# Kernel optimization log

Measured on AMD Instinct MI355X. Metric: run time of the kernel, lower is better.

The kernel has to match this reference:

```python
import jax, jax.numpy as jnp
import numpy as np

OUT = 7   # output_size
SR = 2    # sampling_ratio
SCALES = (0.25, 0.125, 0.0625, 0.03125)  # inferred from feat sizes vs 800x800 image
K_MIN, LVL0, S0, EPS = 2, 4.0, 224.0, 1e-6


def _bilinear_gather(feat, b, y, x):
    """Legacy (aligned=False) bilinear sampling. feat [B,C,H,W]; b,y,x same shape S.
    Returns [*S, C]."""
    B, C, H, W = feat.shape
    valid = (y >= -1.0) & (y <= H) & (x >= -1.0) & (x <= W)
    y = jnp.maximum(y, 0.0)
    x = jnp.maximum(x, 0.0)
    yl = y.astype(jnp.int32)
    xl = x.astype(jnp.int32)
    ycond = yl >= H - 1
    yl = jnp.where(ycond, H - 1, yl)
    yh = jnp.where(ycond, H - 1, yl + 1)
    y = jnp.where(ycond, yl.astype(y.dtype), y)
    xcond = xl >= W - 1
    xl = jnp.where(xcond, W - 1, xl)
    xh = jnp.where(xcond, W - 1, xl + 1)
    x = jnp.where(xcond, xl.astype(x.dtype), x)
    ly = y - yl
    lx = x - xl
    hy = 1.0 - ly
    hx = 1.0 - lx
    def g(yy, xx):
        return feat[b, :, yy, xx]  # advanced indexing -> [*S, C]
    val = ((hy * hx)[..., None] * g(yl, xl)
           + (hy * lx)[..., None] * g(yl, xh)
           + (ly * hx)[..., None] * g(yh, xl)
           + (ly * lx)[..., None] * g(yh, xh))
    return jnp.where(valid[..., None], val, 0.0)


def _roi_align(feat, bidx, boxes, scale):
    """RoIAlign (aligned=False). feat [B,C,H,W], bidx [R] int, boxes [R,4] image coords.
    Returns [R,C,OUT,OUT]."""
    x1 = boxes[:, 0] * scale
    y1 = boxes[:, 1] * scale
    x2 = boxes[:, 2] * scale
    y2 = boxes[:, 3] * scale
    roi_w = jnp.maximum(x2 - x1, 1.0)
    roi_h = jnp.maximum(y2 - y1, 1.0)
    bin_h = roi_h / OUT
    bin_w = roi_w / OUT
    off = (jnp.arange(SR, dtype=feat.dtype) + 0.5) / SR      # [SR]
    ph = jnp.arange(OUT, dtype=feat.dtype)                   # [OUT]
    grid = ph[None, :, None] + off[None, None, :]            # [1,OUT,SR]
    ys = y1[:, None, None] + grid * bin_h[:, None, None]     # [R,OUT,SR]
    xs = x1[:, None, None] + grid * bin_w[:, None, None]     # [R,OUT,SR]
    Y = ys[:, :, None, :, None]                              # [R,OUT,1,SR,1]
    X = xs[:, None, :, None, :]                              # [R,1,OUT,1,SR]
    Yb, Xb = jnp.broadcast_arrays(Y, X)                      # [R,OUT,OUT,SR,SR]
    b = jnp.broadcast_to(bidx[:, None, None, None, None], Yb.shape)
    val = _bilinear_gather(feat, b, Yb, Xb)                  # [R,OUT,OUT,SR,SR,C]
    pooled = val.mean(axis=(3, 4))                           # [R,OUT,OUT,C]
    return jnp.transpose(pooled, (0, 3, 1, 2))               # [R,C,OUT,OUT]


def _levels(boxes_flat):
    """LevelMapper.run: FPN level index (0-based) per RoI."""
    area = (boxes_flat[:, 2] - boxes_flat[:, 0]) * (boxes_flat[:, 3] - boxes_flat[:, 1])
    s = jnp.sqrt(area)
    lvl = jnp.floor(LVL0 + jnp.log2(s / S0 + EPS))
    return jnp.clip(lvl, K_MIN, K_MIN + 3).astype(jnp.int32) - K_MIN


def setup_inputs() -> dict:
    key = jax.random.key(0)
    ks = jax.random.split(key, 6)
    sizes = [200, 100, 50, 25]
    inp = {f"feat{i}": jax.random.normal(ks[i], (2, 256, s, s), dtype=jnp.float32)
           for i, s in enumerate(sizes)}
    xy = jax.random.uniform(ks[4], (2, 256, 2), dtype=jnp.float32) * 500.0
    wh = jax.random.uniform(ks[5], (2, 256, 2), dtype=jnp.float32) * 400.0 + 8.0
    inp["boxes"] = jnp.concatenate([xy, xy + wh], axis=-1)  # (x1,y1,x2,y2) in [0,908)
    return inp


def reference(feat0, feat1, feat2, feat3, boxes):
    feats = [feat0, feat1, feat2, feat3]
    B, N, _ = boxes.shape
    bf = boxes.reshape(B * N, 4)
    bidx = jnp.repeat(jnp.arange(B, dtype=jnp.int32), N)  # convert_to_roi_format ids
    lv = _levels(bf)
    C = feats[0].shape[1]
    out = jnp.zeros((B * N, C, OUT, OUT), dtype=feats[0].dtype)
    for level, (f, sc) in enumerate(zip(feats, SCALES)):
        r = _roi_align(f, bidx, bf, sc)
        out = jnp.where((lv == level)[:, None, None, None], r, out)
    return out
```

## Files before the change

kernel.cpp:

```cpp
#include <hip/hip_runtime.h>

#define OUT 7
#define SR 2
#define NCH 256
#define NB 2
#define NPER 256
#define NROI (NB * NPER)

struct RoiMeta {
    int   level;
    int   bidx;
    float x1, y1;
    float bin_w, bin_h;
};

__global__ void roi_meta_kernel(const float* __restrict__ boxes,
                                RoiMeta* __restrict__ meta) {
    int r = blockIdx.x * blockDim.x + threadIdx.x;
    if (r >= NROI) return;
    float bx1 = boxes[r * 4 + 0];
    float by1 = boxes[r * 4 + 1];
    float bx2 = boxes[r * 4 + 2];
    float by2 = boxes[r * 4 + 3];

    float area = (bx2 - bx1) * (by2 - by1);
    float s    = sqrtf(area);
    float lvl  = floorf(4.0f + log2f(s / 224.0f + 1e-6f));
    lvl        = fminf(fmaxf(lvl, 2.0f), 5.0f);
    int level  = (int)lvl - 2;

    float scale = 0.25f / (float)(1 << level);
    float x1 = bx1 * scale;
    float y1 = by1 * scale;
    float x2 = bx2 * scale;
    float y2 = by2 * scale;
    float roi_w = fmaxf(x2 - x1, 1.0f);
    float roi_h = fmaxf(y2 - y1, 1.0f);

    RoiMeta m;
    m.level = level;
    m.bidx  = r / NPER;
    m.x1    = x1;
    m.y1    = y1;
    m.bin_w = roi_w * (1.0f / OUT);
    m.bin_h = roi_h * (1.0f / OUT);
    meta[r] = m;
}

__device__ __forceinline__ float bilinear_legacy(const float* __restrict__ plane,
                                                 int H, int W, float y, float x) {
    bool valid = (y >= -1.0f) && (y <= (float)H) && (x >= -1.0f) && (x <= (float)W);
    y = fmaxf(y, 0.0f);
    x = fmaxf(x, 0.0f);
    int yl = (int)y;
    int xl = (int)x;
    int yh, xh;
    if (yl >= H - 1) { yl = H - 1; yh = H - 1; y = (float)yl; }
    else             { yh = yl + 1; }
    if (xl >= W - 1) { xl = W - 1; xh = W - 1; x = (float)xl; }
    else             { xh = xl + 1; }
    float ly = y - (float)yl;
    float lx = x - (float)xl;
    float hy = 1.0f - ly;
    float hx = 1.0f - lx;
    const float* rowl = plane + (size_t)yl * W;
    const float* rowh = plane + (size_t)yh * W;
    float v = hy * hx * rowl[xl] + hy * lx * rowl[xh]
            + ly * hx * rowh[xl] + ly * lx * rowh[xh];
    return valid ? v : 0.0f;
}

__global__ void roi_align_kernel(const float* __restrict__ f0,
                                 const float* __restrict__ f1,
                                 const float* __restrict__ f2,
                                 const float* __restrict__ f3,
                                 const RoiMeta* __restrict__ meta,
                                 float* __restrict__ out) {
    int idx = blockIdx.x * blockDim.x + threadIdx.x;
    int pw = idx % OUT;
    int t  = idx / OUT;
    int ph = t % OUT;
    t /= OUT;
    int c = t % NCH;
    int r = t / NCH;
    if (r >= NROI) return;

    RoiMeta m = meta[r];
    const float* f;
    int H;
    switch (m.level) {
        case 0:  f = f0; H = 200; break;
        case 1:  f = f1; H = 100; break;
        case 2:  f = f2; H = 50;  break;
        default: f = f3; H = 25;  break;
    }
    int W = H;
    const float* plane = f + ((size_t)m.bidx * NCH + (size_t)c) * (size_t)H * (size_t)W;

    float acc = 0.0f;
#pragma unroll
    for (int iy = 0; iy < SR; ++iy) {
        float yy = m.y1 + ((float)ph + ((float)iy + 0.5f) * (1.0f / SR)) * m.bin_h;
#pragma unroll
        for (int ix = 0; ix < SR; ++ix) {
            float xx = m.x1 + ((float)pw + ((float)ix + 0.5f) * (1.0f / SR)) * m.bin_w;
            acc += bilinear_legacy(plane, H, W, yy, xx);
        }
    }
    out[idx] = acc * (1.0f / (SR * SR));
}

extern "C" void kernel_launch(void* const* d_in, const int* in_sizes, int n_in,
                              void* d_out, int out_size, void* d_ws, size_t ws_size,
                              hipStream_t stream) {
    const float* f0    = (const float*)d_in[0];
    const float* f1    = (const float*)d_in[1];
    const float* f2    = (const float*)d_in[2];
    const float* f3    = (const float*)d_in[3];
    const float* boxes = (const float*)d_in[4];
    float* out         = (float*)d_out;
    RoiMeta* meta      = (RoiMeta*)d_ws;

    roi_meta_kernel<<<(NROI + 255) / 256, 256, 0, stream>>>(boxes, meta);

    const long long total = (long long)NROI * NCH * OUT * OUT;
    const int block = 256;
    const long long grid = (total + block - 1) / block;
    roi_align_kernel<<<(int)grid, block, 0, stream>>>(f0, f1, f2, f3, meta, out);
}
```

Before: 213.8 us.

## Fuse ROI metadata into align kernel with XCD-aware block mapping and batched loads

Removes the separate metadata kernel and computes each ROI's level, scale and bin sizes inline from the box coordinates, made wave-uniform with readfirstlane. Blocks are remapped so that all blocks of one ROI land on the same XCD (block index mod 8), which should improve L2 reuse of that ROI's feature region. Each block now covers exactly one ROI (TPR divisible by 256). Bilinear weights and offsets are precomputed and all 16 gathers are issued before accumulation to raise memory-level parallelism. Costs are redundant box math per thread and the assumption that the hardware dispatches blocks round-robin across XCDs.

```diff
diff --git a/kernel.cpp b/kernel.cpp
--- a/kernel.cpp
+++ b/kernel.cpp
@@ -1,113 +1,110 @@
 #include <hip/hip_runtime.h>
 
 #define OUT 7
-#define SR 2
 #define NCH 256
 #define NB 2
 #define NPER 256
 #define NROI (NB * NPER)
+#define TPR (NCH * OUT * OUT)
+#define BPR (TPR / 256)
 
-struct RoiMeta {
-    int   level;
-    int   bidx;
-    float x1, y1;
-    float bin_w, bin_h;
-};
+__device__ __forceinline__ float rfl_f(float v) {
+    return __int_as_float(__builtin_amdgcn_readfirstlane(__float_as_int(v)));
+}
 
-__global__ void roi_meta_kernel(const float* __restrict__ boxes,
-                                RoiMeta* __restrict__ meta) {
-    int r = blockIdx.x * blockDim.x + threadIdx.x;
-    if (r >= NROI) return;
-    float bx1 = boxes[r * 4 + 0];
-    float by1 = boxes[r * 4 + 1];
-    float bx2 = boxes[r * 4 + 2];
-    float by2 = boxes[r * 4 + 3];
+__global__ __launch_bounds__(256) void roi_align_kernel(
+        const float* __restrict__ f0, const float* __restrict__ f1,
+        const float* __restrict__ f2, const float* __restrict__ f3,
+        const float* __restrict__ boxes, float* __restrict__ out) {
+    int b    = blockIdx.x;
+    int xcd  = b & 7;
+    int slot = b >> 3;
+    int rr   = slot / BPR;
+    int j    = slot - rr * BPR;
+    int r    = (rr << 3) | xcd;
+
+    int lin = j * 256 + (int)threadIdx.x;
+    int pw  = lin % OUT;
+    int t   = lin / OUT;
+    int ph  = t % OUT;
+    int c   = t / OUT;
+
+    float bx1 = rfl_f(boxes[r * 4 + 0]);
+    float by1 = rfl_f(boxes[r * 4 + 1]);
+    float bx2 = rfl_f(boxes[r * 4 + 2]);
+    float by2 = rfl_f(boxes[r * 4 + 3]);
 
     float area = (bx2 - bx1) * (by2 - by1);
     float s    = sqrtf(area);
-    float lvl  = floorf(4.0f + log2f(s / 224.0f + 1e-6f));
+    float lvl  = floorf(4.0f + log2f(s * (1.0f / 224.0f) + 1e-6f));
     lvl        = fminf(fmaxf(lvl, 2.0f), 5.0f);
-    int level  = (int)lvl - 2;
+    int level  = __builtin_amdgcn_readfirstlane((int)lvl - 2);
 
-    float scale = 0.25f / (float)(1 << level);
+    const float* f;
+    int H;
+    float scale;
+    switch (level) {
+        case 0:  f = f0; H = 200; scale = 0.25f;    break;
+        case 1:  f = f1; H = 100; scale = 0.125f;   break;
+        case 2:  f = f2; H = 50;  scale = 0.0625f;  break;
+        default: f = f3; H = 25;  scale = 0.03125f; break;
+    }
+    float Hf = (float)H;
+
     float x1 = bx1 * scale;
     float y1 = by1 * scale;
-    float x2 = bx2 * scale;
-    float y2 = by2 * scale;
-    float roi_w = fmaxf(x2 - x1, 1.0f);
-    float roi_h = fmaxf(y2 - y1, 1.0f);
+    float roi_w = fmaxf(bx2 * scale - x1, 1.0f);
+    float roi_h = fmaxf(by2 * scale - y1, 1.0f);
+    float bin_w = roi_w * (1.0f / OUT);
+    float bin_h = roi_h * (1.0f / OUT);
 
-    RoiMeta m;
-    m.level = level;
-    m.bidx  = r / NPER;
-    m.x1    = x1;
-    m.y1    = y1;
-    m.bin_w = roi_w * (1.0f / OUT);
-    m.bin_h = roi_h * (1.0f / OUT);
-    meta[r] = m;
-}
+    int bidx = r >> 8;
+    const float* plane = f + (size_t)(bidx * NCH + c) * (size_t)(H * H);
 
-__device__ __forceinline__ float bilinear_legacy(const float* __restrict__ plane,
-                                                 int H, int W, float y, float x) {
-    bool valid = (y >= -1.0f) && (y <= (float)H) && (x >= -1.0f) && (x <= (float)W);
-    y = fmaxf(y, 0.0f);
-    x = fmaxf(x, 0.0f);
-    int yl = (int)y;
-    int xl = (int)x;
-    int yh, xh;
-    if (yl >= H - 1) { yl = H - 1; yh = H - 1; y = (float)yl; }
-    else             { yh = yl + 1; }
-    if (xl >= W - 1) { xl = W - 1; xh = W - 1; x = (float)xl; }
-    else             { xh = xl + 1; }
-    float ly = y - (float)yl;
-    float lx = x - (float)xl;
-    float hy = 1.0f - ly;
-    float hx = 1.0f - lx;
-    const float* rowl = plane + (size_t)yl * W;
-    const float* rowh = plane + (size_t)yh * W;
-    float v = hy * hx * rowl[xl] + hy * lx * rowl[xh]
-            + ly * hx * rowh[xl] + ly * lx * rowh[xh];
-    return valid ? v : 0.0f;
-}
+    float wgt[16];
+    int   off[16];
+#pragma unroll
+    for (int iy = 0; iy < 2; ++iy) {
+        float y   = y1 + ((float)ph + (iy ? 0.75f : 0.25f)) * bin_h;
+        bool  oky = (y >= -1.0f) && (y <= Hf);
+        y = fmaxf(y, 0.0f);
+        int yl = (int)y;
+        int yh;
+        if (yl >= H - 1) { yl = H - 1; yh = H - 1; y = (float)yl; }
+        else             { yh = yl + 1; }
+        float ly = y - (float)yl;
+        float hy = 1.0f - ly;
+        int rl = yl * H;
+        int rh = yh * H;
+#pragma unroll
+        for (int ix = 0; ix < 2; ++ix) {
+            float x  = x1 + ((float)pw + (ix ? 0.75f : 0.25f)) * bin_w;
+            bool  ok = oky && (x >= -1.0f) && (x <= Hf);
+            x = fmaxf(x, 0.0f);
+            int xl = (int)x;
+            int xh;
+            if (xl >= H - 1) { xl = H - 1; xh = H - 1; x = (float)xl; }
+            else             { xh = xl + 1; }
+            float lx = x - (float)xl;
+            float hx = 1.0f - lx;
+            float m  = ok ? 0.25f : 0.0f;
+            int k = (iy * 2 + ix) * 4;
+            wgt[k + 0] = hy * hx * m;  off[k + 0] = rl + xl;
+            wgt[k + 1] = hy * lx * m;  off[k + 1] = rl + xh;
+            wgt[k + 2] = ly * hx * m;  off[k + 2] = rh + xl;
+            wgt[k + 3] = ly * lx * m;  off[k + 3] = rh + xh;
+        }
+    }
 
-__global__ void roi_align_kernel(const float* __restrict__ f0,
-                                 const float* __restrict__ f1,
-                                 const float* __restrict__ f2,
-                                 const float* __restrict__ f3,
-                                 const RoiMeta* __restrict__ meta,
-                                 float* __restrict__ out) {
-    int idx = blockIdx.x * blockDim.x + threadIdx.x;
-    int pw = idx % OUT;
-    int t  = idx / OUT;
-    int ph = t % OUT;
-    t /= OUT;
-    int c = t % NCH;
-    int r = t / NCH;
-    if (r >= NROI) return;
-
-    RoiMeta m = meta[r];
-    const float* f;
-    int H;
-    switch (m.level) {
-        case 0:  f = f0; H = 200; break;
-        case 1:  f = f1; H = 100; break;
-        case 2:  f = f2; H = 50;  break;
-        default: f = f3; H = 25;  break;
-    }
-    int W = H;
-    const float* plane = f + ((size_t)m.bidx * NCH + (size_t)c) * (size_t)H * (size_t)W;
+    float v[16];
+#pragma unroll
+    for (int k = 0; k < 16; ++k) v[k] = plane[off[k]];
 
     float acc = 0.0f;
 #pragma unroll
-    for (int iy = 0; iy < SR; ++iy) {
-        float yy = m.y1 + ((float)ph + ((float)iy + 0.5f) * (1.0f / SR)) * m.bin_h;
-#pragma unroll
-        for (int ix = 0; ix < SR; ++ix) {
-            float xx = m.x1 + ((float)pw + ((float)ix + 0.5f) * (1.0f / SR)) * m.bin_w;
-            acc += bilinear_legacy(plane, H, W, yy, xx);
-        }
-    }
-    out[idx] = acc * (1.0f / (SR * SR));
+    for (int k = 0; k < 16; ++k) acc = fmaf(wgt[k], v[k], acc);
+
+    out[(size_t)r * TPR + lin] = acc;
 }
 
 extern "C" void kernel_launch(void* const* d_in, const int* in_sizes, int n_in,
@@ -119,12 +116,7 @@
     const float* f3    = (const float*)d_in[3];
     const float* boxes = (const float*)d_in[4];
     float* out         = (float*)d_out;
-    RoiMeta* meta      = (RoiMeta*)d_ws;
 
-    roi_meta_kernel<<<(NROI + 255) / 256, 256, 0, stream>>>(boxes, meta);
-
-    const long long total = (long long)NROI * NCH * OUT * OUT;
-    const int block = 256;
-    const long long grid = (total + block - 1) / block;
-    roi_align_kernel<<<(int)grid, block, 0, stream>>>(f0, f1, f2, f3, meta, out);
+    const int grid = NROI * BPR;
+    roi_align_kernel<<<grid, 256, 0, stream>>>(f0, f1, f2, f3, boxes, out);
 }
```

After: 203.4 us. -4.9%, faster.
